# Kernel tuning notes

Measured on AMD Instinct MI355X. Metric: run time of the kernel, lower is better.

The kernel has to match this reference:

```python
import jax, jax.numpy as jnp
import numpy as np

B, LQ, LA = 128, 128, 512
VOCAB, EMB, FILT, K = 50000, 300, 400, 3
EPS = 1e-8


def setup_inputs() -> dict:
    key = jax.random.key(0)
    kq, ka, ke, kw, kb, kW = jax.random.split(key, 6)
    questions = jax.random.randint(kq, (B, LQ), 0, VOCAB + 1, dtype=jnp.int32)
    answers = jax.random.randint(ka, (B, LA), 0, VOCAB + 1, dtype=jnp.int32)
    emb = jax.random.normal(ke, (VOCAB + 1, EMB), dtype=jnp.float32) * 0.1
    emb = emb.at[0].set(0.0)  # padding_idx=0
    fan_in = EMB * K
    bound = 1.0 / np.sqrt(fan_in)
    conv_w = jax.random.uniform(kw, (FILT, EMB, K), jnp.float32, -bound, bound)
    conv_b = jax.random.uniform(kb, (FILT,), jnp.float32, -bound, bound)
    W = jax.random.normal(kW, (FILT, FILT), dtype=jnp.float32)  # init.normal_(std=1)
    return {"questions": questions, "answers": answers, "emb": emb,
            "conv_w": conv_w, "conv_b": conv_b, "W": W}


def _encode(tokens, emb, conv_w, conv_b):
    # tokens [B,L] -> embed [B,L,E] -> transpose to NCH [B,E,L] -> conv1d pad=1
    x = emb[tokens].transpose(0, 2, 1)
    y = jax.lax.conv_general_dilated(
        x, conv_w, window_strides=(1,), padding=[(1, 1)],
        dimension_numbers=("NCH", "OIH", "NCH"))
    return y + conv_b[None, :, None]  # [B, FILT, L]


def reference(questions, answers, emb, conv_w, conv_b, W):
    Q = _encode(questions, emb, conv_w, conv_b)  # [B,F,Lq]
    A = _encode(answers, emb, conv_w, conv_b)    # [B,F,La]
    # G = tanh(Q^T W A)  -> [B, Lq, La]
    G = jnp.tanh(jnp.einsum("bfq,fg,bga->bqa", Q, W, A))
    roQ = jax.nn.softmax(jnp.max(G, axis=2), axis=1)  # [B,Lq]
    roA = jax.nn.softmax(jnp.max(G, axis=1), axis=1)  # [B,La]
    rQ = jnp.einsum("bfq,bq->bf", Q, roQ)  # [B,F]
    rA = jnp.einsum("bfa,ba->bf", A, roA)  # [B,F]
    nQ = jnp.maximum(jnp.linalg.norm(rQ, axis=1), EPS)
    nA = jnp.maximum(jnp.linalg.norm(rA, axis=1), EPS)
    return jnp.sum(rQ * rA, axis=1) / (nQ * nA)  # [B]
```

## Files before the change

kernel.cpp:

```cpp
#include <hip/hip_runtime.h>
#include <hip/hip_bf16.h>

#define BB   128
#define LQ   128
#define LA   512
#define EMBD 300
#define FILT 400
#define KW   3

#define NT   25
#define KC   30
#define KCF  13
#define MT   32

typedef unsigned short u16;
typedef unsigned int   u32;
typedef __attribute__((ext_vector_type(4))) int    i32x4;
typedef __attribute__((ext_vector_type(4))) float  f32x4;
typedef __attribute__((ext_vector_type(8))) __bf16 bf16x8;

__device__ __forceinline__ float b2f(u16 h){ return __uint_as_float(((u32)h) << 16); }
__device__ __forceinline__ u16 f2b(float f){
  u32 u = __float_as_uint(f);
  u32 r = (u + 0x7FFFu + ((u >> 16) & 1u)) >> 16;
  return (u16)r;
}
__device__ __forceinline__ u32 encf(float f){
  u32 u = __float_as_uint(f);
  return (u & 0x80000000u) ? ~u : (u | 0x80000000u);
}
__device__ __forceinline__ float decf(u32 k){
  u32 u = (k & 0x80000000u) ? (k ^ 0x80000000u) : ~k;
  return __uint_as_float(u);
}
__device__ __forceinline__ bf16x8 bzero(){
  i32x4 z; z.x = 0; z.y = 0; z.z = 0; z.w = 0;
  return __builtin_bit_cast(bf16x8, z);
}

__global__ void k_wt2(const float* __restrict__ cw, u32* __restrict__ wTf){
  int idx = blockIdx.x * 256 + threadIdx.x;
  if (idx >= KC * NT * 64) return;
  int kc  = idx / (NT * 64);
  int rem = idx - kc * (NT * 64);
  int nt  = rem >> 6;
  int lane = rem & 63;
  int n = nt * 16 + (lane & 15);
  int quad = lane >> 4;
  u32 pack[4];
  #pragma unroll
  for (int d = 0; d < 4; d++){
    u16 h[2];
    #pragma unroll
    for (int s = 0; s < 2; s++){
      int kp = kc * 32 + quad * 8 + 2 * d + s;
      int kk = kp / 320, e = kp - kk * 320;
      float v = (e < EMBD) ? cw[(size_t)n * (EMBD * KW) + e * KW + kk] : 0.f;
      h[s] = f2b(v);
    }
    pack[d] = (u32)h[0] | ((u32)h[1] << 16);
  }
  i32x4 out4; out4.x = pack[0]; out4.y = pack[1]; out4.z = pack[2]; out4.w = pack[3];
  *((i32x4*)wTf + idx) = out4;
}

__global__ void k_wf(const float* __restrict__ W, u32* __restrict__ wF){
  int idx = blockIdx.x * 256 + threadIdx.x;
  if (idx >= KCF * NT * 64) return;
  int kc  = idx / (NT * 64);
  int rem = idx - kc * (NT * 64);
  int nt  = rem >> 6;
  int lane = rem & 63;
  int n = nt * 16 + (lane & 15);
  int quad = lane >> 4;
  u32 pack[4];
  #pragma unroll
  for (int d = 0; d < 4; d++){
    u16 h[2];
    #pragma unroll
    for (int s = 0; s < 2; s++){
      int k = kc * 32 + quad * 8 + 2 * d + s;
      float v = (k < FILT) ? W[(size_t)k * FILT + n] : 0.f;
      h[s] = f2b(v);
    }
    pack[d] = (u32)h[0] | ((u32)h[1] << 16);
  }
  i32x4 out4; out4.x = pack[0]; out4.y = pack[1]; out4.z = pack[2]; out4.w = pack[3];
  *((i32x4*)wF + idx) = out4;
}

__global__ __launch_bounds__(256) void k_encode_mfma(const int* __restrict__ toks,
    const float* __restrict__ emb, const u32* __restrict__ wTf,
    const float* __restrict__ bias, u16* __restrict__ out, int L){
  __shared__ u16 At[34 * 328];

  const int tid  = threadIdx.x;
  const int w    = tid >> 6;
  const int lane = tid & 63;
  const int col  = lane & 15;
  const int quad = lane >> 4;
  const int half = blockIdx.y;
  const int base_nt = half ? 13 : 0;
  const bool has4 = (half == 0) && (w == 0);
  const int row0 = blockIdx.x * MT;
  const int b    = row0 / L;
  const int l0   = row0 - b * L;

  for (int i = tid; i < 34 * 328 / 2; i += 256) ((u32*)At)[i] = 0u;
  __syncthreads();
  for (int i = tid; i < 34 * 75; i += 256){
    int r = i / 75, c4 = i - r * 75;
    int pos = l0 - 1 + r;
    if ((unsigned)pos < (unsigned)L){
      int t = toks[b * L + pos];
      float4 v = *((const float4*)(emb + (size_t)t * EMBD) + c4);
      u32 p0 = (u32)f2b(v.x) | ((u32)f2b(v.y) << 16);
      u32 p1 = (u32)f2b(v.z) | ((u32)f2b(v.w) << 16);
      int di = (r * 328 + c4 * 4) >> 1;
      ((u32*)At)[di]     = p0;
      ((u32*)At)[di + 1] = p1;
    }
  }

  f32x4 acc[4][2];
  #pragma unroll
  for (int j = 0; j < 4; j++)
    #pragma unroll
    for (int mf = 0; mf < 2; mf++)
      acc[j][mf] = (f32x4){0.f, 0.f, 0.f, 0.f};

  __syncthreads();

  const i32x4* bbase = (const i32x4*)wTf + (size_t)(base_nt + w) * 64 + lane;
  i32x4 Bb[2][4];
  {
    #pragma unroll
    for (int j = 0; j < 3; j++) Bb[0][j] = bbase[(4 * j) * 64];
    if (has4) Bb[0][3] = bbase[12 * 64];
  }
  #pragma unroll
  for (int kc = 0; kc < KC; kc++){
    const int cur = kc & 1;
    if (kc + 1 < KC){
      const i32x4* s = bbase + (size_t)(kc + 1) * (NT * 64);
      #pragma unroll
      for (int j = 0; j < 3; j++) Bb[cur ^ 1][j] = s[(4 * j) * 64];
      if (has4) Bb[cur ^ 1][3] = s[12 * 64];
    }
    const int kk = kc / 10, e0 = (kc - kk * 10) * 32;
    const int ebase = e0 + quad * 8;
    bf16x8 a0 = __builtin_bit_cast(bf16x8, *(const i32x4*)(At + (col + kk) * 328 + ebase));
    bf16x8 a1 = __builtin_bit_cast(bf16x8, *(const i32x4*)(At + (16 + col + kk) * 328 + ebase));
    #pragma unroll
    for (int j = 0; j < 3; j++){
      bf16x8 bf = __builtin_bit_cast(bf16x8, Bb[cur][j]);
      acc[j][0] = __builtin_amdgcn_mfma_f32_16x16x32_bf16(a0, bf, acc[j][0], 0, 0, 0);
      acc[j][1] = __builtin_amdgcn_mfma_f32_16x16x32_bf16(a1, bf, acc[j][1], 0, 0, 0);
    }
    if (has4){
      bf16x8 bf = __builtin_bit_cast(bf16x8, Bb[cur][3]);
      acc[3][0] = __builtin_amdgcn_mfma_f32_16x16x32_bf16(a0, bf, acc[3][0], 0, 0, 0);
      acc[3][1] = __builtin_amdgcn_mfma_f32_16x16x32_bf16(a1, bf, acc[3][1], 0, 0, 0);
    }
  }

  #pragma unroll
  for (int j = 0; j < 4; j++){
    if (j == 3 && !has4) continue;
    int n = (base_nt + w + 4 * j) * 16 + col;
    float bv = bias[n];
    #pragma unroll
    for (int mf = 0; mf < 2; mf++){
      int rbase = row0 + mf * 16 + quad * 4;
      #pragma unroll
      for (int r = 0; r < 4; r++)
        out[(size_t)(rbase + r) * FILT + n] = f2b(acc[j][mf][r] + bv);
    }
  }
}

__global__ __launch_bounds__(256) void k_gemmT2(const u16* __restrict__ QT,
    const u32* __restrict__ wF, u16* __restrict__ T){
  const int tid  = threadIdx.x;
  const int w    = tid >> 6;
  const int lane = tid & 63;
  const int col  = lane & 15;
  const int quad = lane >> 4;
  const int row0 = blockIdx.x * MT;

  f32x4 acc[7][2];
  #pragma unroll
  for (int j = 0; j < 7; j++)
    #pragma unroll
    for (int mf = 0; mf < 2; mf++)
      acc[j][mf] = (f32x4){0.f, 0.f, 0.f, 0.f};

  const u16* arow0 = QT + (size_t)(row0 + col) * FILT;
  const u16* arow1 = QT + (size_t)(row0 + 16 + col) * FILT;
  const i32x4* bbase = (const i32x4*)wF + lane;

  i32x4 Ab[2][2];
  i32x4 Bb[2][7];
  {
    int off = quad * 8;
    Ab[0][0] = *(const i32x4*)(arow0 + off);
    Ab[0][1] = *(const i32x4*)(arow1 + off);
    #pragma unroll
    for (int j = 0; j < 6; j++) Bb[0][j] = bbase[(w + 4 * j) * 64];
    if (w == 0) Bb[0][6] = bbase[24 * 64];
  }
  #pragma unroll
  for (int kc = 0; kc < KCF; kc++){
    const int cur = kc & 1;
    if (kc + 1 < KCF){
      int off = (kc + 1) * 32 + quad * 8;
      Ab[cur ^ 1][0] = *(const i32x4*)(arow0 + off);
      Ab[cur ^ 1][1] = *(const i32x4*)(arow1 + off);
      const i32x4* s = bbase + (size_t)(kc + 1) * (NT * 64);
      #pragma unroll
      for (int j = 0; j < 6; j++) Bb[cur ^ 1][j] = s[(w + 4 * j) * 64];
      if (w == 0) Bb[cur ^ 1][6] = s[24 * 64];
    }
    bf16x8 a0 = __builtin_bit_cast(bf16x8, Ab[cur][0]);
    bf16x8 a1 = __builtin_bit_cast(bf16x8, Ab[cur][1]);
    #pragma unroll
    for (int j = 0; j < 6; j++){
      bf16x8 bf = __builtin_bit_cast(bf16x8, Bb[cur][j]);
      acc[j][0] = __builtin_amdgcn_mfma_f32_16x16x32_bf16(a0, bf, acc[j][0], 0, 0, 0);
      acc[j][1] = __builtin_amdgcn_mfma_f32_16x16x32_bf16(a1, bf, acc[j][1], 0, 0, 0);
    }
    if (w == 0){
      bf16x8 bf = __builtin_bit_cast(bf16x8, Bb[cur][6]);
      acc[6][0] = __builtin_amdgcn_mfma_f32_16x16x32_bf16(a0, bf, acc[6][0], 0, 0, 0);
      acc[6][1] = __builtin_amdgcn_mfma_f32_16x16x32_bf16(a1, bf, acc[6][1], 0, 0, 0);
    }
  }

  #pragma unroll
  for (int j = 0; j < 7; j++){
    if (j == 6 && w != 0) continue;
    int nt = (j < 6) ? (w + 4 * j) : 24;
    int n = nt * 16 + col;
    #pragma unroll
    for (int mf = 0; mf < 2; mf++){
      int rbase = row0 + mf * 16 + quad * 4;
      #pragma unroll
      for (int r = 0; r < 4; r++)
        T[(size_t)(rbase + r) * FILT + n] = f2b(acc[j][mf][r]);
    }
  }
}

__global__ __launch_bounds__(256) void k_scores2(const u16* __restrict__ T,
    const u16* __restrict__ AT, u32* __restrict__ rowmaxE, float* __restrict__ colmax){
  __shared__ float rpart[128][17];
  __shared__ float cpart[128][17];
  const int tid  = threadIdx.x;
  const int w    = tid >> 6;
  const int lane = tid & 63;
  const int col  = lane & 15;
  const int quad = lane >> 4;
  const int b    = blockIdx.y;
  const int a0   = blockIdx.x * 128;

  f32x4 acc[2][8];
  #pragma unroll
  for (int i = 0; i < 2; i++)
    #pragma unroll
    for (int j = 0; j < 8; j++)
      acc[i][j] = (f32x4){0.f, 0.f, 0.f, 0.f};

  const u16* tr0 = T  + (size_t)(b * LQ + (2 * w) * 16 + col) * FILT;
  const u16* tr1 = T  + (size_t)(b * LQ + (2 * w + 1) * 16 + col) * FILT;
  const u16* ar  = AT + (size_t)(b * LA + a0 + col) * FILT;

  i32x4 Abuf[2][2], Bbuf[2][8];
  {
    int off = quad * 8;
    Abuf[0][0] = *(const i32x4*)(tr0 + off);
    Abuf[0][1] = *(const i32x4*)(tr1 + off);
    #pragma unroll
    for (int j = 0; j < 8; j++)
      Bbuf[0][j] = *(const i32x4*)(ar + (size_t)(j * 16) * FILT + off);
  }
  #pragma unroll
  for (int kc = 0; kc < KCF; kc++){
    const int cur = kc & 1;
    if (kc + 1 < KCF){
      int off = (kc + 1) * 32 + quad * 8;
      Abuf[cur ^ 1][0] = *(const i32x4*)(tr0 + off);
      Abuf[cur ^ 1][1] = *(const i32x4*)(tr1 + off);
      #pragma unroll
      for (int j = 0; j < 8; j++)
        Bbuf[cur ^ 1][j] = *(const i32x4*)(ar + (size_t)(j * 16) * FILT + off);
    }
    const bool live = (kc < 12) || (quad < 2);
    bf16x8 a0 = live ? __builtin_bit_cast(bf16x8, Abuf[cur][0]) : bzero();
    bf16x8 a1 = live ? __builtin_bit_cast(bf16x8, Abuf[cur][1]) : bzero();
    #pragma unroll
    for (int j = 0; j < 8; j++){
      bf16x8 bf = __builtin_bit_cast(bf16x8, Bbuf[cur][j]);
      acc[0][j] = __builtin_amdgcn_mfma_f32_16x16x32_bf16(a0, bf, acc[0][j], 0, 0, 0);
      acc[1][j] = __builtin_amdgcn_mfma_f32_16x16x32_bf16(a1, bf, acc[1][j], 0, 0, 0);
    }
  }

  #pragma unroll
  for (int i = 0; i < 2; i++)
    #pragma unroll
    for (int r = 0; r < 4; r++){
      float m = acc[i][0][r];
      #pragma unroll
      for (int j = 1; j < 8; j++) m = fmaxf(m, acc[i][j][r]);
      rpart[(2 * w + i) * 16 + quad * 4 + r][col] = m;
    }
  #pragma unroll
  for (int j = 0; j < 8; j++){
    float m = acc[0][j][0];
    #pragma unroll
    for (int i = 0; i < 2; i++)
      #pragma unroll
      for (int r = 0; r < 4; r++) m = fmaxf(m, acc[i][j][r]);
    cpart[j * 16 + col][w * 4 + quad] = m;
  }
  __syncthreads();
  if (tid < 128){
    float m = rpart[tid][0];
    #pragma unroll
    for (int g = 1; g < 16; g++) m = fmaxf(m, rpart[tid][g]);
    atomicMax(&rowmaxE[b * LQ + tid], encf(m));
    float m2 = cpart[tid][0];
    #pragma unroll
    for (int g = 1; g < 16; g++) m2 = fmaxf(m2, cpart[tid][g]);
    colmax[b * LA + a0 + tid] = m2;
  }
}

__global__ __launch_bounds__(256) void k_soft(const u32* __restrict__ rme,
    const float* __restrict__ cm, float* __restrict__ roq, float* __restrict__ roa){
  __shared__ float sq[128];
  __shared__ float sa[512];
  __shared__ float red[4];
  int b = blockIdx.x, tid = threadIdx.x;
  if (tid < 128) sq[tid] = tanhf(decf(rme[b * LQ + tid]));
  sa[tid]       = tanhf(cm[b * LA + tid]);
  sa[tid + 256] = tanhf(cm[b * LA + 256 + tid]);
  __syncthreads();
  if (tid < 64){
    float m = fmaxf(sq[tid], sq[tid + 64]);
    #pragma unroll
    for (int off = 32; off; off >>= 1) m = fmaxf(m, __shfl_down(m, off));
    if (tid == 0) red[0] = m;
  } else if (tid < 128){
    int l = tid - 64;
    float m = sa[l];
    #pragma unroll
    for (int i = 1; i < 8; i++) m = fmaxf(m, sa[l + 64 * i]);
    #pragma unroll
    for (int off = 32; off; off >>= 1) m = fmaxf(m, __shfl_down(m, off));
    if (l == 0) red[1] = m;
  }
  __syncthreads();
  float mq = red[0], ma = red[1];
  if (tid < 128) sq[tid] = __expf(sq[tid] - mq);
  sa[tid]       = __expf(sa[tid] - ma);
  sa[tid + 256] = __expf(sa[tid + 256] - ma);
  __syncthreads();
  if (tid < 64){
    float s = sq[tid] + sq[tid + 64];
    #pragma unroll
    for (int off = 32; off; off >>= 1) s += __shfl_down(s, off);
    if (tid == 0) red[2] = s;
  } else if (tid < 128){
    int l = tid - 64;
    float s = 0.f;
    #pragma unroll
    for (int i = 0; i < 8; i++) s += sa[l + 64 * i];
    #pragma unroll
    for (int off = 32; off; off >>= 1) s += __shfl_down(s, off);
    if (l == 0) red[3] = s;
  }
  __syncthreads();
  float iq = 1.f / red[2], ia = 1.f / red[3];
  if (tid < 128) roq[b * LQ + tid] = sq[tid] * iq;
  roa[b * LA + tid]       = sa[tid] * ia;
  roa[b * LA + 256 + tid] = sa[tid + 256] * ia;
}

__global__ __launch_bounds__(256) void k_pool(const u16* __restrict__ QT,
    const u16* __restrict__ AT, const float* __restrict__ roq, const float* __restrict__ roa,
    float* __restrict__ rqp, float* __restrict__ rap){
  __shared__ float wq[32];
  __shared__ float wa[128];
  int s = blockIdx.x, b = blockIdx.y, tid = threadIdx.x;
  if (tid < 32) wq[tid] = roq[b * LQ + s * 32 + tid];
  if (tid >= 128 && tid < 256) wa[tid - 128] = roa[b * LA + s * 128 + (tid - 128)];
  __syncthreads();
  if (tid < FILT / 2){
    const u32* qp = (const u32*)(QT + (size_t)(b * LQ + s * 32) * FILT) + tid;
    const u32* ap = (const u32*)(AT + (size_t)(b * LA + s * 128) * FILT) + tid;
    float rq0 = 0.f, rq1 = 0.f, ra0 = 0.f, ra1 = 0.f;
    for (int q = 0; q < 32; q++){
      u32 u = qp[q * (FILT / 2)];
      float wv = wq[q];
      rq0 += __uint_as_float(u << 16) * wv;
      rq1 += __uint_as_float(u & 0xFFFF0000u) * wv;
    }
    for (int a = 0; a < 128; a++){
      u32 u = ap[a * (FILT / 2)];
      float wv = wa[a];
      ra0 += __uint_as_float(u << 16) * wv;
      ra1 += __uint_as_float(u & 0xFFFF0000u) * wv;
    }
    size_t base = ((size_t)b * 4 + s) * FILT + 2 * tid;
    rqp[base] = rq0; rqp[base + 1] = rq1;
    rap[base] = ra0; rap[base + 1] = ra1;
  }
}

__global__ __launch_bounds__(256) void k_cos(const float* __restrict__ rqp,
    const float* __restrict__ rap, float* __restrict__ outp){
  __shared__ float rd[4], r1[4], r2[4];
  int b = blockIdx.x, tid = threadIdx.x;
  int lane = tid & 63, w = tid >> 6;
  float d = 0.f, n1 = 0.f, n2 = 0.f;
  for (int f = tid; f < FILT; f += 256){
    size_t base = (size_t)b * 4 * FILT + f;
    float rq = rqp[base] + rqp[base + FILT] + rqp[base + 2 * FILT] + rqp[base + 3 * FILT];
    float ra = rap[base] + rap[base + FILT] + rap[base + 2 * FILT] + rap[base + 3 * FILT];
    d += rq * ra; n1 += rq * rq; n2 += ra * ra;
  }
  #pragma unroll
  for (int off = 32; off; off >>= 1){
    d  += __shfl_down(d, off);
    n1 += __shfl_down(n1, off);
    n2 += __shfl_down(n2, off);
  }
  if (lane == 0){ rd[w] = d; r1[w] = n1; r2[w] = n2; }
  __syncthreads();
  if (tid == 0){
    float D  = rd[0] + rd[1] + rd[2] + rd[3];
    float N1 = r1[0] + r1[1] + r1[2] + r1[3];
    float N2 = r2[0] + r2[1] + r2[2] + r2[3];
    outp[b] = D / (fmaxf(sqrtf(N1), 1e-8f) * fmaxf(sqrtf(N2), 1e-8f));
  }
}

extern "C" void kernel_launch(void* const* d_in, const int* in_sizes, int n_in,
                              void* d_out, int out_size, void* d_ws, size_t ws_size,
                              hipStream_t stream){
  const int*   qtok = (const int*)d_in[0];
  const int*   atok = (const int*)d_in[1];
  const float* emb  = (const float*)d_in[2];
  const float* cw   = (const float*)d_in[3];
  const float* cb   = (const float*)d_in[4];
  const float* W    = (const float*)d_in[5];
  float* outp = (float*)d_out;

  char* ws = (char*)d_ws;
  size_t off = 0;
  auto alloc = [&](size_t bytes) -> char* {
    char* p = ws + off;
    off = (off + bytes + 255) & ~(size_t)255;
    return p;
  };
  u32*   wTf = (u32*)alloc((size_t)KC * NT * 64 * 16);
  u32*   wF  = (u32*)alloc((size_t)KCF * NT * 64 * 16);
  u16*   QT  = (u16*)alloc((size_t)BB * LQ * FILT * 2);
  u16*   AT  = (u16*)alloc((size_t)BB * LA * FILT * 2);
  u16*   T   = (u16*)alloc((size_t)BB * LQ * FILT * 2);
  u32*   rme = (u32*)alloc((size_t)BB * LQ * 4);
  float* cm  = (float*)alloc((size_t)BB * LA * 4);
  float* roq = (float*)alloc((size_t)BB * LQ * 4);
  float* roa = (float*)alloc((size_t)BB * LA * 4);
  float* rqp = (float*)alloc((size_t)BB * 4 * FILT * 4);
  float* rap = (float*)alloc((size_t)BB * 4 * FILT * 4);

  hipMemsetAsync(rme, 0, (size_t)BB * LQ * 4, stream);

  k_wt2<<<dim3((KC * NT * 64 + 255) / 256), 256, 0, stream>>>(cw, wTf);
  k_wf<<<dim3((KCF * NT * 64 + 255) / 256), 256, 0, stream>>>(W, wF);
  k_encode_mfma<<<dim3(BB * LQ / MT, 2), 256, 0, stream>>>(qtok, emb, wTf, cb, QT, LQ);
  k_encode_mfma<<<dim3(BB * LA / MT, 2), 256, 0, stream>>>(atok, emb, wTf, cb, AT, LA);
  k_gemmT2<<<dim3(BB * LQ / MT), 256, 0, stream>>>(QT, wF, T);
  k_scores2<<<dim3(LA / 128, BB), 256, 0, stream>>>(T, AT, rme, cm);
  k_soft<<<dim3(BB), 256, 0, stream>>>(rme, cm, roq, roa);
  k_pool<<<dim3(4, BB), 256, 0, stream>>>(QT, AT, roq, roa, rqp, rap);
  k_cos<<<dim3(BB), 256, 0, stream>>>(rqp, rap, outp);
}
```

Baseline: 275.0 us.

## Split gemmT and scores kernels across more blocks; prefetch LDS A-operand in encode

The encode kernel now double-buffers its shared-memory A-fragment reads one step ahead, like the B loads. k_gemmT is split into two blocks along the filter dimension, each doing 13 or 12 N-tiles, which matches the encode kernel's layout. k_scores is split in two along the question dimension: each warp handles one 16-row Q tile, and the column max is merged across blocks with atomicMax on an encoded float, which needs an extra memset. Together these double the grid size and cut per-thread register pressure, at the cost of reloading the A/B operands twice and adding atomics.

```diff
diff --git a/kernel.cpp b/kernel.cpp
--- a/kernel.cpp
+++ b/kernel.cpp
@@ -133,10 +133,14 @@
 
   const i32x4* bbase = (const i32x4*)wTf + (size_t)(base_nt + w) * 64 + lane;
   i32x4 Bb[2][4];
+  i32x4 Ab[2][2];
   {
     #pragma unroll
     for (int j = 0; j < 3; j++) Bb[0][j] = bbase[(4 * j) * 64];
     if (has4) Bb[0][3] = bbase[12 * 64];
+    const int ebase0 = quad * 8;
+    Ab[0][0] = *(const i32x4*)(At + (col) * 328 + ebase0);
+    Ab[0][1] = *(const i32x4*)(At + (16 + col) * 328 + ebase0);
   }
   #pragma unroll
   for (int kc = 0; kc < KC; kc++){
@@ -146,11 +150,13 @@
       #pragma unroll
       for (int j = 0; j < 3; j++) Bb[cur ^ 1][j] = s[(4 * j) * 64];
       if (has4) Bb[cur ^ 1][3] = s[12 * 64];
-    }
-    const int kk = kc / 10, e0 = (kc - kk * 10) * 32;
-    const int ebase = e0 + quad * 8;
-    bf16x8 a0 = __builtin_bit_cast(bf16x8, *(const i32x4*)(At + (col + kk) * 328 + ebase));
-    bf16x8 a1 = __builtin_bit_cast(bf16x8, *(const i32x4*)(At + (16 + col + kk) * 328 + ebase));
+      const int kk1 = (kc + 1) / 10, e01 = ((kc + 1) - kk1 * 10) * 32;
+      const int ebase1 = e01 + quad * 8;
+      Ab[cur ^ 1][0] = *(const i32x4*)(At + (col + kk1) * 328 + ebase1);
+      Ab[cur ^ 1][1] = *(const i32x4*)(At + (16 + col + kk1) * 328 + ebase1);
+    }
+    bf16x8 a0 = __builtin_bit_cast(bf16x8, Ab[cur][0]);
+    bf16x8 a1 = __builtin_bit_cast(bf16x8, Ab[cur][1]);
     #pragma unroll
     for (int j = 0; j < 3; j++){
       bf16x8 bf = __builtin_bit_cast(bf16x8, Bb[cur][j]);
@@ -179,35 +185,38 @@
   }
 }
 
-__global__ __launch_bounds__(256) void k_gemmT2(const u16* __restrict__ QT,
+__global__ __launch_bounds__(256) void k_gemmT3(const u16* __restrict__ QT,
     const u32* __restrict__ wF, u16* __restrict__ T){
   const int tid  = threadIdx.x;
   const int w    = tid >> 6;
   const int lane = tid & 63;
   const int col  = lane & 15;
   const int quad = lane >> 4;
+  const int half = blockIdx.y;
+  const int base_nt = half ? 13 : 0;
+  const bool has4 = (half == 0) && (w == 0);
   const int row0 = blockIdx.x * MT;
 
-  f32x4 acc[7][2];
-  #pragma unroll
-  for (int j = 0; j < 7; j++)
+  f32x4 acc[4][2];
+  #pragma unroll
+  for (int j = 0; j < 4; j++)
     #pragma unroll
     for (int mf = 0; mf < 2; mf++)
       acc[j][mf] = (f32x4){0.f, 0.f, 0.f, 0.f};
 
   const u16* arow0 = QT + (size_t)(row0 + col) * FILT;
   const u16* arow1 = QT + (size_t)(row0 + 16 + col) * FILT;
-  const i32x4* bbase = (const i32x4*)wF + lane;
+  const i32x4* bbase = (const i32x4*)wF + (size_t)(base_nt + w) * 64 + lane;
 
   i32x4 Ab[2][2];
-  i32x4 Bb[2][7];
+  i32x4 Bb[2][4];
   {
     int off = quad * 8;
     Ab[0][0] = *(const i32x4*)(arow0 + off);
     Ab[0][1] = *(const i32x4*)(arow1 + off);
     #pragma unroll
-    for (int j = 0; j < 6; j++) Bb[0][j] = bbase[(w + 4 * j) * 64];
-    if (w == 0) Bb[0][6] = bbase[24 * 64];
+    for (int j = 0; j < 3; j++) Bb[0][j] = bbase[(4 * j) * 64];
+    if (has4) Bb[0][3] = bbase[12 * 64];
   }
   #pragma unroll
   for (int kc = 0; kc < KCF; kc++){
@@ -218,29 +227,28 @@
       Ab[cur ^ 1][1] = *(const i32x4*)(arow1 + off);
       const i32x4* s = bbase + (size_t)(kc + 1) * (NT * 64);
       #pragma unroll
-      for (int j = 0; j < 6; j++) Bb[cur ^ 1][j] = s[(w + 4 * j) * 64];
-      if (w == 0) Bb[cur ^ 1][6] = s[24 * 64];
+      for (int j = 0; j < 3; j++) Bb[cur ^ 1][j] = s[(4 * j) * 64];
+      if (has4) Bb[cur ^ 1][3] = s[12 * 64];
     }
     bf16x8 a0 = __builtin_bit_cast(bf16x8, Ab[cur][0]);
     bf16x8 a1 = __builtin_bit_cast(bf16x8, Ab[cur][1]);
     #pragma unroll
-    for (int j = 0; j < 6; j++){
+    for (int j = 0; j < 3; j++){
       bf16x8 bf = __builtin_bit_cast(bf16x8, Bb[cur][j]);
       acc[j][0] = __builtin_amdgcn_mfma_f32_16x16x32_bf16(a0, bf, acc[j][0], 0, 0, 0);
       acc[j][1] = __builtin_amdgcn_mfma_f32_16x16x32_bf16(a1, bf, acc[j][1], 0, 0, 0);
     }
-    if (w == 0){
-      bf16x8 bf = __builtin_bit_cast(bf16x8, Bb[cur][6]);
-      acc[6][0] = __builtin_amdgcn_mfma_f32_16x16x32_bf16(a0, bf, acc[6][0], 0, 0, 0);
-      acc[6][1] = __builtin_amdgcn_mfma_f32_16x16x32_bf16(a1, bf, acc[6][1], 0, 0, 0);
-    }
-  }
-
-  #pragma unroll
-  for (int j = 0; j < 7; j++){
-    if (j == 6 && w != 0) continue;
-    int nt = (j < 6) ? (w + 4 * j) : 24;
-    int n = nt * 16 + col;
+    if (has4){
+      bf16x8 bf = __builtin_bit_cast(bf16x8, Bb[cur][3]);
+      acc[3][0] = __builtin_amdgcn_mfma_f32_16x16x32_bf16(a0, bf, acc[3][0], 0, 0, 0);
+      acc[3][1] = __builtin_amdgcn_mfma_f32_16x16x32_bf16(a1, bf, acc[3][1], 0, 0, 0);
+    }
+  }
+
+  #pragma unroll
+  for (int j = 0; j < 4; j++){
+    if (j == 3 && !has4) continue;
+    int n = (base_nt + w + 4 * j) * 16 + col;
     #pragma unroll
     for (int mf = 0; mf < 2; mf++){
       int rbase = row0 + mf * 16 + quad * 4;
@@ -251,9 +259,9 @@
   }
 }
 
-__global__ __launch_bounds__(256) void k_scores2(const u16* __restrict__ T,
-    const u16* __restrict__ AT, u32* __restrict__ rowmaxE, float* __restrict__ colmax){
-  __shared__ float rpart[128][17];
+__global__ __launch_bounds__(256) void k_scores3(const u16* __restrict__ T,
+    const u16* __restrict__ AT, u32* __restrict__ rowmaxE, u32* __restrict__ colmaxE){
+  __shared__ float rpart[64][17];
   __shared__ float cpart[128][17];
   const int tid  = threadIdx.x;
   const int w    = tid >> 6;
@@ -262,23 +270,19 @@
   const int quad = lane >> 4;
   const int b    = blockIdx.y;
   const int a0   = blockIdx.x * 128;
-
-  f32x4 acc[2][8];
-  #pragma unroll
-  for (int i = 0; i < 2; i++)
-    #pragma unroll
-    for (int j = 0; j < 8; j++)
-      acc[i][j] = (f32x4){0.f, 0.f, 0.f, 0.f};
-
-  const u16* tr0 = T  + (size_t)(b * LQ + (2 * w) * 16 + col) * FILT;
-  const u16* tr1 = T  + (size_t)(b * LQ + (2 * w + 1) * 16 + col) * FILT;
-  const u16* ar  = AT + (size_t)(b * LA + a0 + col) * FILT;
-
-  i32x4 Abuf[2][2], Bbuf[2][8];
+  const int qt   = blockIdx.z * 4 + w;
+
+  f32x4 acc[8];
+  #pragma unroll
+  for (int j = 0; j < 8; j++) acc[j] = (f32x4){0.f, 0.f, 0.f, 0.f};
+
+  const u16* tr = T  + (size_t)(b * LQ + qt * 16 + col) * FILT;
+  const u16* ar = AT + (size_t)(b * LA + a0 + col) * FILT;
+
+  i32x4 Abuf[2], Bbuf[2][8];
   {
     int off = quad * 8;
-    Abuf[0][0] = *(const i32x4*)(tr0 + off);
-    Abuf[0][1] = *(const i32x4*)(tr1 + off);
+    Abuf[0] = *(const i32x4*)(tr + off);
     #pragma unroll
     for (int j = 0; j < 8; j++)
       Bbuf[0][j] = *(const i32x4*)(ar + (size_t)(j * 16) * FILT + off);
@@ -288,63 +292,65 @@
     const int cur = kc & 1;
     if (kc + 1 < KCF){
       int off = (kc + 1) * 32 + quad * 8;
-      Abuf[cur ^ 1][0] = *(const i32x4*)(tr0 + off);
-      Abuf[cur ^ 1][1] = *(const i32x4*)(tr1 + off);
+      Abuf[cur ^ 1] = *(const i32x4*)(tr + off);
       #pragma unroll
       for (int j = 0; j < 8; j++)
         Bbuf[cur ^ 1][j] = *(const i32x4*)(ar + (size_t)(j * 16) * FILT + off);
     }
     const bool live = (kc < 12) || (quad < 2);
-    bf16x8 a0 = live ? __builtin_bit_cast(bf16x8, Abuf[cur][0]) : bzero();
-    bf16x8 a1 = live ? __builtin_bit_cast(bf16x8, Abuf[cur][1]) : bzero();
+    bf16x8 a0 = live ? __builtin_bit_cast(bf16x8, Abuf[cur]) : bzero();
     #pragma unroll
     for (int j = 0; j < 8; j++){
       bf16x8 bf = __builtin_bit_cast(bf16x8, Bbuf[cur][j]);
-      acc[0][j] = __builtin_amdgcn_mfma_f32_16x16x32_bf16(a0, bf, acc[0][j], 0, 0, 0);
-      acc[1][j] = __builtin_amdgcn_mfma_f32_16x16x32_bf16(a1, bf, acc[1][j], 0, 0, 0);
-    }
-  }
-
-  #pragma unroll
-  for (int i = 0; i < 2; i++)
-    #pragma unroll
-    for (int r = 0; r < 4; r++){
-      float m = acc[i][0][r];
-      #pragma unroll
-      for (int j = 1; j < 8; j++) m = fmaxf(m, acc[i][j][r]);
-      rpart[(2 * w + i) * 16 + quad * 4 + r][col] = m;
-    }
+      acc[j] = __builtin_amdgcn_mfma_f32_16x16x32_bf16(a0, bf, acc[j], 0, 0, 0);
+    }
+  }
+
+  #pragma unroll
+  for (int r = 0; r < 4; r++){
+    float m = acc[0][r];
+    #pragma unroll
+    for (int j = 1; j < 8; j++) m = fmaxf(m, acc[j][r]);
+    rpart[w * 16 + quad * 4 + r][col] = m;
+  }
   #pragma unroll
   for (int j = 0; j < 8; j++){
-    float m = acc[0][j][0];
-    #pragma unroll
-    for (int i = 0; i < 2; i++)
-      #pragma unroll
-      for (int r = 0; r < 4; r++) m = fmaxf(m, acc[i][j][r]);
+    float m = acc[j][0];
+    #pragma unroll
+    for (int r = 1; r < 4; r++) m = fmaxf(m, acc[j][r]);
     cpart[j * 16 + col][w * 4 + quad] = m;
   }
   __syncthreads();
-  if (tid < 128){
+  if (tid < 64){
     float m = rpart[tid][0];
     #pragma unroll
     for (int g = 1; g < 16; g++) m = fmaxf(m, rpart[tid][g]);
-    atomicMax(&rowmaxE[b * LQ + tid], encf(m));
-    float m2 = cpart[tid][0];
-    #pragma unroll
-    for (int g = 1; g < 16; g++) m2 = fmaxf(m2, cpart[tid][g]);
-    colmax[b * LA + a0 + tid] = m2;
+    atomicMax(&rowmaxE[b * LQ + blockIdx.z * 64 + tid], encf(m));
+  } else if (tid < 192){
+    int a = tid - 64;
+    float m2 = cpart[a][0];
+    #pragma unroll
+    for (int g = 1; g < 16; g++) m2 = fmaxf(m2, cpart[a][g]);
+    atomicMax(&colmaxE[b * LA + a0 + a], encf(m2));
+  }
+  if (tid >= 192 && tid < 256){
+    int a = tid - 128;
+    float m2 = cpart[a][0];
+    #pragma unroll
+    for (int g = 1; g < 16; g++) m2 = fmaxf(m2, cpart[a][g]);
+    atomicMax(&colmaxE[b * LA + a0 + a], encf(m2));
   }
 }
 
 __global__ __launch_bounds__(256) void k_soft(const u32* __restrict__ rme,
-    const float* __restrict__ cm, float* __restrict__ roq, float* __restrict__ roa){
+    const u32* __restrict__ cme, float* __restrict__ roq, float* __restrict__ roa){
   __shared__ float sq[128];
   __shared__ float sa[512];
   __shared__ float red[4];
   int b = blockIdx.x, tid = threadIdx.x;
   if (tid < 128) sq[tid] = tanhf(decf(rme[b * LQ + tid]));
-  sa[tid]       = tanhf(cm[b * LA + tid]);
-  sa[tid + 256] = tanhf(cm[b * LA + 256 + tid]);
+  sa[tid]       = tanhf(decf(cme[b * LA + tid]));
+  sa[tid + 256] = tanhf(decf(cme[b * LA + 256 + tid]));
   __syncthreads();
   if (tid < 64){
     float m = fmaxf(sq[tid], sq[tid + 64]);
@@ -470,21 +476,22 @@
   u16*   AT  = (u16*)alloc((size_t)BB * LA * FILT * 2);
   u16*   T   = (u16*)alloc((size_t)BB * LQ * FILT * 2);
   u32*   rme = (u32*)alloc((size_t)BB * LQ * 4);
-  float* cm  = (float*)alloc((size_t)BB * LA * 4);
+  u32*   cme = (u32*)alloc((size_t)BB * LA * 4);
   float* roq = (float*)alloc((size_t)BB * LQ * 4);
   float* roa = (float*)alloc((size_t)BB * LA * 4);
   float* rqp = (float*)alloc((size_t)BB * 4 * FILT * 4);
   float* rap = (float*)alloc((size_t)BB * 4 * FILT * 4);
 
   hipMemsetAsync(rme, 0, (size_t)BB * LQ * 4, stream);
+  hipMemsetAsync(cme, 0, (size_t)BB * LA * 4, stream);
 
   k_wt2<<<dim3((KC * NT * 64 + 255) / 256), 256, 0, stream>>>(cw, wTf);
   k_wf<<<dim3((KCF * NT * 64 + 255) / 256), 256, 0, stream>>>(W, wF);
   k_encode_mfma<<<dim3(BB * LQ / MT, 2), 256, 0, stream>>>(qtok, emb, wTf, cb, QT, LQ);
   k_encode_mfma<<<dim3(BB * LA / MT, 2), 256, 0, stream>>>(atok, emb, wTf, cb, AT, LA);
-  k_gemmT2<<<dim3(BB * LQ / MT), 256, 0, stream>>>(QT, wF, T);
-  k_scores2<<<dim3(LA / 128, BB), 256, 0, stream>>>(T, AT, rme, cm);
-  k_soft<<<dim3(BB), 256, 0, stream>>>(rme, cm, roq, roa);
+  k_gemmT3<<<dim3(BB * LQ / MT, 2), 256, 0, stream>>>(QT, wF, T);
+  k_scores3<<<dim3(LA / 128, BB, 2), 256, 0, stream>>>(T, AT, rme, cme);
+  k_soft<<<dim3(BB), 256, 0, stream>>>(rme, cme, roq, roa);
   k_pool<<<dim3(4, BB), 256, 0, stream>>>(QT, AT, roq, roa, rqp, rap);
   k_cos<<<dim3(BB), 256, 0, stream>>>(rqp, rap, outp);
 }
```

Measured after the change: 285.7 us. +3.9%, slower.
